# Kernel optimization log

Measured on AMD Instinct MI355X. Metric: run time of the kernel, lower is better.

## Reference

```python
import jax, jax.numpy as jnp
import numpy as np

NUM_HEADS = 16
WINDOW = 128
PERSIST = 16


def setup_inputs() -> dict:
    key = jax.random.key(0)
    ks = jax.random.split(key, 6)
    B, S, D, L = 2, 2048, 2048, 512
    sd = 1.0 / np.sqrt(D)
    sl = 1.0 / np.sqrt(L)
    return {
        "x": jax.random.normal(ks[0], (B, S, D), dtype=jnp.float32),
        "Wq": jax.random.normal(ks[1], (D, D), dtype=jnp.float32) * sd,
        "Wkv": jax.random.normal(ks[2], (D, L), dtype=jnp.float32) * sd,
        "Wk": jax.random.normal(ks[3], (L, D), dtype=jnp.float32) * sl,
        "Wv": jax.random.normal(ks[4], (L, D), dtype=jnp.float32) * sl,
        "Wo": jax.random.normal(ks[5], (D, D), dtype=jnp.float32) * sd,
    }


def reference(x, Wq, Wkv, Wk, Wv, Wo):
    B, S, D = x.shape
    H = NUM_HEADS
    hd = D // H
    scale = hd ** -0.5

    q = (x @ Wq).reshape(B, S, H, hd)
    kv_latent = x @ Wkv                      # MLA-style latent bottleneck
    k = (kv_latent @ Wk).reshape(B, S, H, hd)
    v = (kv_latent @ Wv).reshape(B, S, H, hd)

    # causal + sliding-window + persistent attention-sink mask
    qi = jnp.arange(S)[:, None]
    ki = jnp.arange(S)[None, :]
    mask = (ki <= qi) & ((qi - ki < WINDOW) | (ki < PERSIST))  # [S,S]

    scores = jnp.einsum("bqhd,bkhd->bhqk", q, k) * scale
    scores = jnp.where(mask[None, None], scores, jnp.finfo(scores.dtype).min)
    attn = jax.nn.softmax(scores, axis=-1)
    out = jnp.einsum("bhqk,bkhd->bqhd", attn, v).reshape(B, S, D)
    return out @ Wo
```

## Files before the change

kernel.cpp:

```cpp
#include <hip/hip_runtime.h>

typedef float f32x4 __attribute__((ext_vector_type(4)));
typedef __bf16 bf16x8 __attribute__((ext_vector_type(8)));

__device__ __forceinline__ short f2bf(float f) {
    union { float f; unsigned u; } x; x.f = f;
    unsigned r = x.u + 0x7fffu + ((x.u >> 16) & 1u);
    return (short)(r >> 16);
}

__device__ __forceinline__ void store_out(float* p, float v) { *p = v; }
__device__ __forceinline__ void store_out(short* p, float v) { *p = f2bf(v); }

__device__ __forceinline__ void gload_lds16(const short* g, short* l) {
    __builtin_amdgcn_global_load_lds(
        (__attribute__((address_space(1))) void*)(void*)g,
        (__attribute__((address_space(3))) void*)l, 16, 0, 0);
}

__global__ void prep_all(const float* __restrict__ x, short* __restrict__ xb,
                         const float* __restrict__ Wq, const float* __restrict__ Wo,
                         const float* __restrict__ Wk, const float* __restrict__ Wv,
                         const float* __restrict__ Wkv,
                         short* __restrict__ WqkvT, short* __restrict__ WoT,
                         short* __restrict__ WkT, short* __restrict__ WvT) {
    __shared__ float tile[32][33];
    int id = blockIdx.x;
    const int t = threadIdx.x;
    if (id < 8192) {
        const int i = id * 256 + t;
        float4 v = ((const float4*)x)[i];
        ((short4*)xb)[i] = make_short4(f2bf(v.x), f2bf(v.y), f2bf(v.z), f2bf(v.w));
        return;
    }
    id -= 8192;
    const float* in; short* out; int R, C, xt, yt;
    if (id < 4096)       { in = Wq;  out = WqkvT; R = 2048; C = 2048; xt = id & 63; yt = id >> 6; }
    else if (id < 8192)  { id -= 4096; in = Wo;  out = WoT;  R = 2048; C = 2048; xt = id & 63; yt = id >> 6; }
    else if (id < 9216)  { id -= 8192; in = Wk;  out = WkT;  R = 512;  C = 2048; xt = id & 63; yt = id >> 6; }
    else if (id < 10240) { id -= 9216; in = Wv;  out = WvT;  R = 512;  C = 2048; xt = id & 63; yt = id >> 6; }
    else                 { id -= 10240; in = Wkv; out = WqkvT + (size_t)2048 * 2048;
                           R = 2048; C = 512; xt = id & 15; yt = id >> 4; }
    const int c0 = xt * 32, r0 = yt * 32;
    const int tx = t & 31, ty = t >> 5;
#pragma unroll
    for (int i = 0; i < 32; i += 8)
        tile[ty + i][tx] = in[(size_t)(r0 + ty + i) * C + c0 + tx];
    __syncthreads();
#pragma unroll
    for (int i = 0; i < 32; i += 8)
        out[(size_t)(c0 + ty + i) * R + r0 + tx] = f2bf(tile[tx][ty + i]);
}

#define MFMA16(a, b, c) __builtin_amdgcn_mfma_f32_16x16x32_bf16(a, b, c, 0, 0, 0)

#define LBASE(buf, kh, ab) ((((((buf) << 1) | (kh)) << 1) | (ab)) * 8192)

#define STAGE(P, ld, tt, kh, buf, ab)                                   \
    do {                                                                \
        const int kb_ = (tt) * 64 + (kh) * 32;                          \
        const short* s_ = (P) + kb_;                                    \
        short* d_ = lds + LBASE(buf, kh, ab) + w * 512;                 \
        gload_lds16(s_, d_);                                            \
        gload_lds16(s_ + (size_t)128 * (ld), d_ + 4096);                \
    } while (0)

#define VM6 asm volatile("s_waitcnt vmcnt(6)" ::: "memory")

#define MM_ROW(mi, areg)                                                \
    acc[mi][0] = MFMA16(areg, bv0, acc[mi][0]);                         \
    acc[mi][1] = MFMA16(areg, bv1, acc[mi][1]);                         \
    acc[mi][2] = MFMA16(areg, bv2, acc[mi][2]);                         \
    acc[mi][3] = MFMA16(areg, bv3, acc[mi][3]);

#define HALFK(buf, kh, STG0, W0, STG1)                                  \
    {                                                                   \
        bf16x8 bv0, bv1, bv2, bv3;                                      \
        {                                                               \
            const short* Ab_ = lds + LBASE(buf, kh, 0) + (wm * 128) * 32 + foff; \
            const short* Bb_ = lds + LBASE(buf, kh, 1) + (wn * 64) * 32 + foff;  \
            bf16x8 a0_ = *(const bf16x8*)&Ab_[0];                       \
            bf16x8 a1_ = *(const bf16x8*)&Ab_[512];                     \
            bf16x8 a2_ = *(const bf16x8*)&Ab_[1024];                    \
            bf16x8 a3_ = *(const bf16x8*)&Ab_[1536];                    \
            bv0 = *(const bf16x8*)&Bb_[0];                              \
            bv1 = *(const bf16x8*)&Bb_[512];                            \
            bv2 = *(const bf16x8*)&Bb_[1024];                           \
            bv3 = *(const bf16x8*)&Bb_[1536];                           \
            STG0;                                                       \
            W0;                                                         \
            __builtin_amdgcn_s_barrier();                               \
            asm volatile("s_waitcnt lgkmcnt(0)" ::: "memory");          \
            __builtin_amdgcn_sched_barrier(0);                          \
            __builtin_amdgcn_s_setprio(1);                              \
            MM_ROW(0, a0_) MM_ROW(1, a1_) MM_ROW(2, a2_) MM_ROW(3, a3_) \
            __builtin_amdgcn_s_setprio(0);                              \
            __builtin_amdgcn_s_barrier();                               \
        }                                                               \
        {                                                               \
            const short* Ab_ = lds + LBASE(buf, kh, 0) + (wm * 128 + 64) * 32 + foff; \
            bf16x8 a0_ = *(const bf16x8*)&Ab_[0];                       \
            bf16x8 a1_ = *(const bf16x8*)&Ab_[512];                     \
            bf16x8 a2_ = *(const bf16x8*)&Ab_[1024];                    \
            bf16x8 a3_ = *(const bf16x8*)&Ab_[1536];                    \
            STG1;                                                       \
            __builtin_amdgcn_s_barrier();                               \
            asm volatile("s_waitcnt lgkmcnt(0)" ::: "memory");          \
            __builtin_amdgcn_sched_barrier(0);                          \
            __builtin_amdgcn_s_setprio(1);                              \
            MM_ROW(4, a0_) MM_ROW(5, a1_) MM_ROW(6, a2_) MM_ROW(7, a3_) \
            __builtin_amdgcn_s_setprio(0);                              \
            __builtin_amdgcn_s_barrier();                               \
        }                                                               \
    }

template <typename OutT>
__device__ __forceinline__ void gemm256_core(
    const short* __restrict__ A, const short* __restrict__ Bt, OutT* __restrict__ C,
    int m0, int n0, int K, int lda, int ldb, int ldc, short* lds) {
    const int t = threadIdx.x;
    const int w = t >> 6, l = t & 63;
    const int wm = w >> 2, wn = w & 3;
    const int l15 = l & 15, lc = l >> 4;

    const int su = (l & 7) ^ ((l >> 3) & 7);
    const int srow = (w << 4) + ((l >> 3) << 1) + (su >> 2);
    const int scol = (su & 3) << 3;
    const short* Ag = A + (size_t)(m0 + srow) * lda + scol;
    const short* Bg = Bt + (size_t)(n0 + srow) * ldb + scol;

    const int i3 = ((((l15 & 1) << 2) | lc) ^ ((l15 >> 1) & 7));
    const int foff = (l15 >> 1) * 64 + i3 * 8;

    f32x4 acc[8][4] = {};

    const int ntm1 = (K >> 6) - 1;
    const int niter = K >> 7;

    STAGE(Ag, lda, 0, 0, 0, 0);
    STAGE(Bg, ldb, 0, 0, 0, 1);
    STAGE(Ag, lda, 0, 1, 0, 0);
    STAGE(Bg, ldb, 0, 1, 0, 1);
    STAGE(Ag, lda, 1, 0, 1, 0);
    STAGE(Bg, ldb, 1, 0, 1, 1);
    asm volatile("s_waitcnt vmcnt(8)" ::: "memory");
    __builtin_amdgcn_s_barrier();

#pragma unroll 1
    for (int it = 0; it < niter; ++it) {
        const int tt = it * 2;
        const int t1 = tt + 1;
        const int t2 = (tt + 2 > ntm1) ? ntm1 : tt + 2;
        const int t3 = (tt + 3 > ntm1) ? ntm1 : tt + 3;
        HALFK(0, 0, STAGE(Ag, lda, t1, 1, 1, 0), VM6, STAGE(Bg, ldb, t1, 1, 1, 1))
        HALFK(0, 1, STAGE(Ag, lda, t2, 0, 0, 0), VM6, STAGE(Bg, ldb, t2, 0, 0, 1))
        HALFK(1, 0, STAGE(Ag, lda, t2, 1, 0, 0), VM6, STAGE(Bg, ldb, t2, 1, 0, 1))
        HALFK(1, 1, STAGE(Ag, lda, t3, 0, 1, 0), VM6, STAGE(Bg, ldb, t3, 0, 1, 1))
    }

    asm volatile("s_waitcnt vmcnt(0)" ::: "memory");

    const int crow = m0 + wm * 128 + lc * 4;
    const int ccol = n0 + wn * 64 + l15;
#pragma unroll
    for (int mi = 0; mi < 8; ++mi)
#pragma unroll
        for (int ni = 0; ni < 4; ++ni) {
            OutT* cp = C + (size_t)(crow + mi * 16) * ldc + ccol + ni * 16;
#pragma unroll
            for (int rr = 0; rr < 4; ++rr)
                store_out(cp + (size_t)rr * ldc, acc[mi][ni][rr]);
        }
}

__global__ __launch_bounds__(512, 2)
void gemm256_kv(const short* __restrict__ kvl, const short* __restrict__ WkT,
                short* __restrict__ kk, const short* __restrict__ WvT,
                short* __restrict__ vT) {
    extern __shared__ short lds[];
    int id = blockIdx.x;
    if (id < 128) {
        gemm256_core<short>(kvl, WkT, kk, (id >> 3) * 256, (id & 7) * 256,
                            512, 2560, 512, 2048, lds);
    } else {
        id -= 128;
        gemm256_core<short>(WvT, kvl, vT, (id >> 4) * 256, (id & 15) * 256,
                            512, 512, 2560, 4096, lds);
    }
}

#define LQ(s) ((s) * 13312)

#define QSTG(ps, pt)                                                    \
    do {                                                                \
        const int kb_ = (pt) * 32;                                      \
        gload_lds16(Ag + kb_, lds + LQ(ps) + w * 512);                  \
        gload_lds16(Ag + kb_ + (size_t)128 * lda, lds + LQ(ps) + 4096 + w * 512); \
        gload_lds16(Bg + kb_, lds + LQ(ps) + 8192 + w * 512);           \
        if (w < 2)                                                      \
            gload_lds16(Bh + kb_, lds + LQ(ps) + 12288 + w * 512);      \
    } while (0)

#define QPH(s, ps, pt)                                                  \
    {                                                                   \
        const short* Ab_ = lds + LQ(s) + wm * 2048 + foff;              \
        const short* Bb_ = lds + LQ(s) + 8192 + wn * 2560 + foff;       \
        bf16x8 a0_ = *(const bf16x8*)&Ab_[0];                           \
        bf16x8 a1_ = *(const bf16x8*)&Ab_[512];                         \
        bf16x8 a2_ = *(const bf16x8*)&Ab_[1024];                        \
        bf16x8 a3_ = *(const bf16x8*)&Ab_[1536];                        \
        bf16x8 b0_ = *(const bf16x8*)&Bb_[0];                           \
        bf16x8 b1_ = *(const bf16x8*)&Bb_[512];                         \
        bf16x8 b2_ = *(const bf16x8*)&Bb_[1024];                        \
        bf16x8 b3_ = *(const bf16x8*)&Bb_[1536];                        \
        bf16x8 b4_ = *(const bf16x8*)&Bb_[2048];                        \
        QSTG(ps, pt);                                                   \
        asm volatile("s_waitcnt vmcnt(8)" ::: "memory");                \
        __builtin_amdgcn_s_barrier();                                   \
        asm volatile("s_waitcnt lgkmcnt(0)" ::: "memory");              \
        __builtin_amdgcn_sched_barrier(0);                              \
        __builtin_amdgcn_s_setprio(1);                                  \
        acc[0][0]=MFMA16(a0_,b0_,acc[0][0]); acc[0][1]=MFMA16(a0_,b1_,acc[0][1]); \
        acc[0][2]=MFMA16(a0_,b2_,acc[0][2]); acc[0][3]=MFMA16(a0_,b3_,acc[0][3]); \
        acc[0][4]=MFMA16(a0_,b4_,acc[0][4]);                            \
        acc[1][0]=MFMA16(a1_,b0_,acc[1][0]); acc[1][1]=MFMA16(a1_,b1_,acc[1][1]); \
        acc[1][2]=MFMA16(a1_,b2_,acc[1][2]); acc[1][3]=MFMA16(a1_,b3_,acc[1][3]); \
        acc[1][4]=MFMA16(a1_,b4_,acc[1][4]);                            \
        acc[2][0]=MFMA16(a2_,b0_,acc[2][0]); acc[2][1]=MFMA16(a2_,b1_,acc[2][1]); \
        acc[2][2]=MFMA16(a2_,b2_,acc[2][2]); acc[2][3]=MFMA16(a2_,b3_,acc[2][3]); \
        acc[2][4]=MFMA16(a2_,b4_,acc[2][4]);                            \
        acc[3][0]=MFMA16(a3_,b0_,acc[3][0]); acc[3][1]=MFMA16(a3_,b1_,acc[3][1]); \
        acc[3][2]=MFMA16(a3_,b2_,acc[3][2]); acc[3][3]=MFMA16(a3_,b3_,acc[3][3]); \
        acc[3][4]=MFMA16(a3_,b4_,acc[3][4]);                            \
        __builtin_amdgcn_s_setprio(0);                                  \
        __builtin_amdgcn_s_barrier();                                   \
    }

__global__ __launch_bounds__(512, 1)
void gemm_qkv160(const short* __restrict__ A, const short* __restrict__ Bt,
                 short* __restrict__ C, int K, int lda, int ldb, int ldc) {
    extern __shared__ short lds[];
    const int sw = ((int)blockIdx.x & 7) * 32 + ((int)blockIdx.x >> 3);
    const int m0 = (sw >> 4) * 256, n0 = (sw & 15) * 160;
    const int t = threadIdx.x;
    const int w = t >> 6, l = t & 63;
    const int wm = w >> 1, wn = w & 1;
    const int l15 = l & 15, lc = l >> 4;

    const int su = (l & 7) ^ ((l >> 3) & 7);
    const int srow = (w << 4) + ((l >> 3) << 1) + (su >> 2);
    const int scol = (su & 3) << 3;
    const short* Ag = A + (size_t)(m0 + srow) * lda + scol;
    const short* Bg = Bt + (size_t)(n0 + srow) * ldb + scol;
    const short* Bh = Bt + (size_t)(n0 + 128 + srow) * ldb + scol;

    const int i3 = ((((l15 & 1) << 2) | lc) ^ ((l15 >> 1) & 7));
    const int foff = (l15 >> 1) * 64 + i3 * 8;

    f32x4 acc[4][5] = {};
    const int last = (K >> 5) - 1;

    QSTG(0, 0); QSTG(1, 1); QSTG(2, 2);
    asm volatile("s_waitcnt vmcnt(6)" ::: "memory");
    __builtin_amdgcn_s_barrier();

#pragma unroll 1
    for (int it = 0; it < (K >> 7); ++it) {
        const int h0 = it * 4;
        const int q3 = h0 + 3;
        const int q4 = (h0 + 4 > last) ? last : h0 + 4;
        const int q5 = (h0 + 5 > last) ? last : h0 + 5;
        const int q6 = (h0 + 6 > last) ? last : h0 + 6;
        QPH(0, 3, q3)
        QPH(1, 0, q4)
        QPH(2, 1, q5)
        QPH(3, 2, q6)
    }
    asm volatile("s_waitcnt vmcnt(0)" ::: "memory");

    const int crow = m0 + wm * 64 + lc * 4;
    const int ccol = n0 + wn * 80 + l15;
#pragma unroll
    for (int mi = 0; mi < 4; ++mi)
#pragma unroll
        for (int ni = 0; ni < 5; ++ni) {
            short* cp = C + (size_t)(crow + mi * 16) * ldc + ccol + ni * 16;
#pragma unroll
            for (int rr = 0; rr < 4; ++rr)
                store_out(cp + (size_t)rr * ldc, acc[mi][ni][rr]);
        }
}

#define LB2(s) ((s) * 12288)

#define STG2(ps, pt)                                                    \
    do {                                                                \
        const int kb_ = (pt) * 32;                                      \
        gload_lds16(Ag + kb_, lds + LB2(ps) + w * 512);                 \
        gload_lds16(Ag + kb_ + (size_t)128 * lda, lds + LB2(ps) + 4096 + w * 512); \
        gload_lds16(Bg + kb_, lds + LB2(ps) + 8192 + w * 512);          \
    } while (0)

#define PH2(s, ps, pt)                                                  \
    {                                                                   \
        const short* Ab_ = lds + LB2(s) + wm * 2048 + foff;             \
        const short* Bb_ = lds + LB2(s) + 8192 + wn * 2048 + foff;      \
        bf16x8 a0_ = *(const bf16x8*)&Ab_[0];                           \
        bf16x8 a1_ = *(const bf16x8*)&Ab_[512];                         \
        bf16x8 a2_ = *(const bf16x8*)&Ab_[1024];                        \
        bf16x8 a3_ = *(const bf16x8*)&Ab_[1536];                        \
        bf16x8 b0_ = *(const bf16x8*)&Bb_[0];                           \
        bf16x8 b1_ = *(const bf16x8*)&Bb_[512];                         \
        bf16x8 b2_ = *(const bf16x8*)&Bb_[1024];                        \
        bf16x8 b3_ = *(const bf16x8*)&Bb_[1536];                        \
        STG2(ps, pt);                                                   \
        asm volatile("s_waitcnt vmcnt(6)" ::: "memory");                \
        __builtin_amdgcn_s_barrier();                                   \
        asm volatile("s_waitcnt lgkmcnt(0)" ::: "memory");              \
        __builtin_amdgcn_sched_barrier(0);                              \
        __builtin_amdgcn_s_setprio(1);                                  \
        acc[0][0]=MFMA16(a0_,b0_,acc[0][0]); acc[0][1]=MFMA16(a0_,b1_,acc[0][1]); \
        acc[0][2]=MFMA16(a0_,b2_,acc[0][2]); acc[0][3]=MFMA16(a0_,b3_,acc[0][3]); \
        acc[1][0]=MFMA16(a1_,b0_,acc[1][0]); acc[1][1]=MFMA16(a1_,b1_,acc[1][1]); \
        acc[1][2]=MFMA16(a1_,b2_,acc[1][2]); acc[1][3]=MFMA16(a1_,b3_,acc[1][3]); \
        acc[2][0]=MFMA16(a2_,b0_,acc[2][0]); acc[2][1]=MFMA16(a2_,b1_,acc[2][1]); \
        acc[2][2]=MFMA16(a2_,b2_,acc[2][2]); acc[2][3]=MFMA16(a2_,b3_,acc[2][3]); \
        acc[3][0]=MFMA16(a3_,b0_,acc[3][0]); acc[3][1]=MFMA16(a3_,b1_,acc[3][1]); \
        acc[3][2]=MFMA16(a3_,b2_,acc[3][2]); acc[3][3]=MFMA16(a3_,b3_,acc[3][3]); \
        __builtin_amdgcn_s_setprio(0);                                  \
        __builtin_amdgcn_s_barrier();                                   \
    }

__global__ __launch_bounds__(512, 1)
void gemm_out(const short* __restrict__ A, const short* __restrict__ Bt,
              float* __restrict__ C, int K, int lda, int ldb, int ldc) {
    extern __shared__ short lds[];
    const int sw = ((int)blockIdx.x & 7) * 32 + ((int)blockIdx.x >> 3);
    const int m0 = (sw >> 4) * 256, n0 = (sw & 15) * 128;
    const int t = threadIdx.x;
    const int w = t >> 6, l = t & 63;
    const int wm = w >> 1, wn = w & 1;
    const int l15 = l & 15, lc = l >> 4;

    const int su = (l & 7) ^ ((l >> 3) & 7);
    const int srow = (w << 4) + ((l >> 3) << 1) + (su >> 2);
    const int scol = (su & 3) << 3;
    const short* Ag = A + (size_t)(m0 + srow) * lda + scol;
    const short* Bg = Bt + (size_t)(n0 + srow) * ldb + scol;

    const int i3 = ((((l15 & 1) << 2) | lc) ^ ((l15 >> 1) & 7));
    const int foff = (l15 >> 1) * 64 + i3 * 8;

    f32x4 acc[4][4] = {};

    const int nkh1 = (K >> 5) - 1;

    STG2(0, 0);
    STG2(1, 1);
    STG2(2, 2);
    asm volatile("s_waitcnt vmcnt(6)" ::: "memory");
    __builtin_amdgcn_s_barrier();

#pragma unroll 1
    for (int it = 0; it < (K >> 7); ++it) {
        const int h0 = it * 4;
        const int p3 = h0 + 3;
        const int p4 = (h0 + 4 > nkh1) ? nkh1 : h0 + 4;
        const int p5 = (h0 + 5 > nkh1) ? nkh1 : h0 + 5;
        const int p6 = (h0 + 6 > nkh1) ? nkh1 : h0 + 6;
        PH2(0, 3, p3)
        PH2(1, 0, p4)
        PH2(2, 1, p5)
        PH2(3, 2, p6)
    }

    asm volatile("s_waitcnt vmcnt(0)" ::: "memory");

    const int crow = m0 + wm * 64 + lc * 4;
    const int ccol = n0 + wn * 64 + l15;
#pragma unroll
    for (int mi = 0; mi < 4; ++mi)
#pragma unroll
        for (int ni = 0; ni < 4; ++ni) {
            float* cp = C + (size_t)(crow + mi * 16) * ldc + ccol + ni * 16;
#pragma unroll
            for (int rr = 0; rr < 4; ++rr)
                store_out(cp + (size_t)rr * ldc, acc[mi][ni][rr]);
        }
}

#define A_S 2048
#define A_D 2048
#define A_M 4096
#define A_HD 128
__global__ __launch_bounds__(256)
void attn_win3(const short* __restrict__ Q, const short* __restrict__ K,
               const short* __restrict__ vT, short* __restrict__ O, int ldq) {
    const int qt = blockIdx.x, h = blockIdx.y, b = blockIdx.z;
    const int Qs = qt * 64;
    const int t = threadIdx.x, w = t >> 6, l = t & 63;
    const int qs = Qs + w * 16;
    const int lg = l >> 4, ln = l & 15;
    const float SCALE = 0.088388347648318447f;

    __shared__ __align__(16) short sK[2][512 * 8];
    __shared__ __align__(16) short sV[2][512 * 8];
    __shared__ __align__(16) short sP[4][16][40];

    const size_t bS = (size_t)b * A_S;
    const short* qrow = Q + (bS + qs + ln) * ldq + h * A_HD;
    bf16x8 qf[4];
#pragma unroll
    for (int ks = 0; ks < 4; ++ks)
        qf[ks] = *(const bf16x8*)(qrow + ks * 32 + lg * 8);

    f32x4 o[8] = {};
    float lsum[4] = {0.f, 0.f, 0.f, 0.f};

    int C_lo = (Qs - 127) >> 5; if (C_lo < 0) C_lo = 0;
    const int C_hi = (Qs + 63) >> 5;
    const bool sink = C_lo > 0;
    const int total = (C_hi - C_lo + 1) + (sink ? 1 : 0);

    const int key0 = t >> 4, dseg0s = (t & 15) ^ (key0 & 7);
    const int d0 = t >> 2, ksg0 = (t & 3) ^ ((d0 >> 1) & 3);
    const int key1 = (256 + t) >> 4, dseg1s = (t & 15) ^ (key1 & 7);
    const int d1 = (256 + t) >> 2, ksg1 = (t & 3) ^ ((d1 >> 1) & 3);
    const short* Kb = K + bS * A_D + h * A_HD;
    const short* Vb = vT + (size_t)h * A_HD * A_M + b * A_S;

#define ASTAGE(kb, buf)                                                         \
    do {                                                                        \
        gload_lds16(Kb + (size_t)((kb) + key0) * A_D + dseg0s * 8,              \
                    &sK[buf][(size_t)(w * 64) * 8]);                            \
        gload_lds16(Vb + (size_t)d0 * A_M + (kb) + ksg0 * 8,                    \
                    &sV[buf][(size_t)(w * 64) * 8]);                            \
        gload_lds16(Kb + (size_t)((kb) + key1) * A_D + dseg1s * 8,              \
                    &sK[buf][(size_t)(256 + w * 64) * 8]);                      \
        gload_lds16(Vb + (size_t)d1 * A_M + (kb) + ksg1 * 8,                    \
                    &sV[buf][(size_t)(256 + w * 64) * 8]);                      \
    } while (0)

#define CHUNK_KB(ci) ((((sink) && (ci) == 0) ? 0 : (C_lo + (ci) - (sink ? 1 : 0))) * 32)

    ASTAGE(CHUNK_KB(0), 0);
    __syncthreads();

    for (int ci = 0; ci < total; ++ci) {
        if (ci + 1 < total) {
            const int nkb = CHUNK_KB(ci + 1);
            ASTAGE(nkb, (ci + 1) & 1);
        }
        const int kb = CHUNK_KB(ci);
        const int buf = ci & 1;
        const bool any = (kb < 16) || ((kb + 31 >= qs - 127) && (kb <= qs + 15));
        if (any) {
            f32x4 s0 = {0.f, 0.f, 0.f, 0.f}, s1 = {0.f, 0.f, 0.f, 0.f};
#pragma unroll
            for (int ks = 0; ks < 4; ++ks) {
                const int dsg = ks * 4 + lg;
                bf16x8 k0 = *(const bf16x8*)&sK[buf][(ln * 16 + (dsg ^ (ln & 7))) * 8];
                bf16x8 k1 = *(const bf16x8*)&sK[buf][((16 + ln) * 16 + (dsg ^ (ln & 7))) * 8];
                s0 = __builtin_amdgcn_mfma_f32_16x16x32_bf16(qf[ks], k0, s0, 0, 0, 0);
                s1 = __builtin_amdgcn_mfma_f32_16x16x32_bf16(qf[ks], k1, s1, 0, 0, 0);
            }
            const int k0i = kb + ln, k1i = kb + 16 + ln;
#pragma unroll
            for (int r = 0; r < 4; ++r) {
                const int qi = qs + lg * 4 + r;
                const bool m0 = (k0i <= qi) && ((qi - k0i < 128) || (k0i < 16));
                const bool m1 = (k1i <= qi) && ((qi - k1i < 128) || (k1i < 16));
                const float p0 = m0 ? __expf(s0[r] * SCALE) : 0.f;
                const float p1 = m1 ? __expf(s1[r] * SCALE) : 0.f;
                lsum[r] += p0 + p1;
                sP[w][lg * 4 + r][ln] = f2bf(p0);
                sP[w][lg * 4 + r][16 + ln] = f2bf(p1);
            }
            bf16x8 pf = *(const bf16x8*)&sP[w][ln][lg * 8];
#pragma unroll
            for (int dgi = 0; dgi < 8; ++dgi) {
                const int d = dgi * 16 + ln;
                bf16x8 vf = *(const bf16x8*)&sV[buf][(d * 4 + (lg ^ ((ln >> 1) & 3))) * 8];
                o[dgi] = __builtin_amdgcn_mfma_f32_16x16x32_bf16(pf, vf, o[dgi], 0, 0, 0);
            }
        }
        __syncthreads();
    }
#undef ASTAGE
#undef CHUNK_KB

#pragma unroll
    for (int r = 0; r < 4; ++r) {
        float s = lsum[r];
        s += __shfl_xor(s, 1); s += __shfl_xor(s, 2);
        s += __shfl_xor(s, 4); s += __shfl_xor(s, 8);
        const float inv = 1.0f / s;
        short* orow = O + (bS + qs + lg * 4 + r) * A_D + h * A_HD + ln;
#pragma unroll
        for (int dgi = 0; dgi < 8; ++dgi)
            orow[dgi * 16] = f2bf(o[dgi][r] * inv);
    }
}

extern "C" void kernel_launch(void* const* d_in, const int* in_sizes, int n_in,
                              void* d_out, int out_size, void* d_ws, size_t ws_size,
                              hipStream_t stream) {
    (void)in_sizes; (void)n_in; (void)out_size; (void)ws_size;
    const float* x   = (const float*)d_in[0];
    const float* Wq  = (const float*)d_in[1];
    const float* Wkv = (const float*)d_in[2];
    const float* Wk  = (const float*)d_in[3];
    const float* Wv  = (const float*)d_in[4];
    const float* Wo  = (const float*)d_in[5];
    float* out = (float*)d_out;

    const int B = 2, S = 2048, D = 2048, L = 512, H = 16;
    const int M = B * S;
    const int NQ = D + L;

    short* p = (short*)d_ws;
    short* xb    = p; p += (size_t)M * D;
    short* WqkvT = p; p += (size_t)NQ * D;
    short* WkT   = p; p += (size_t)D * L;
    short* WvT   = p; p += (size_t)D * L;
    short* WoT   = p; p += (size_t)D * D;
    short* qkv   = p; p += (size_t)M * NQ;
    short* kk    = p; p += (size_t)M * D;
    short* vT    = p; p += (size_t)D * M;
    short* ao    = p; p += (size_t)M * D;

    static bool attr_done = false;
    if (!attr_done) {
        hipFuncSetAttribute((const void*)&gemm256_kv,
                            hipFuncAttributeMaxDynamicSharedMemorySize, 131072);
        hipFuncSetAttribute((const void*)&gemm_qkv160,
                            hipFuncAttributeMaxDynamicSharedMemorySize, 106496);
        hipFuncSetAttribute((const void*)&gemm_out,
                            hipFuncAttributeMaxDynamicSharedMemorySize, 98304);
        attr_done = true;
    }

    prep_all<<<19456, 256, 0, stream>>>(x, xb, Wq, Wo, Wk, Wv, Wkv,
                                        WqkvT, WoT, WkT, WvT);
    gemm_qkv160<<<256, 512, 106496, stream>>>(xb, WqkvT, qkv, D, D, D, NQ);
    gemm256_kv<<<256, 512, 131072, stream>>>(qkv + D, WkT, kk, WvT, vT);

    attn_win3<<<dim3(S / 64, H, B), 256, 0, stream>>>(qkv, kk, vT, ao, NQ);

    gemm_out<<<256, 512, 98304, stream>>>(ao, WoT, out, D, D, D, D);
}
```

Measured before the change: 254.8 us.

## Move Wo transpose into attention kernel tail and drop explicit LDS waits

The Wo fp32-to-bf16 transpose leaves the prep kernel and is done by extra blocks appended to the attention grid (qt>=32), so it overlaps with the lightly loaded attention work. This is meant to shorten the serial prep phase. Separately, the explicit lgkmcnt(0) wait and sched_barrier before the MFMA bursts in two GEMM macros are removed, which leaves the compiler to schedule the LDS-read waits. That could allow better interleaving but may change ordering around the barrier.

```diff
diff --git a/kernel.cpp b/kernel.cpp
--- a/kernel.cpp
+++ b/kernel.cpp
@@ -19,10 +19,10 @@
 }
 
 __global__ void prep_all(const float* __restrict__ x, short* __restrict__ xb,
-                         const float* __restrict__ Wq, const float* __restrict__ Wo,
+                         const float* __restrict__ Wq,
                          const float* __restrict__ Wk, const float* __restrict__ Wv,
                          const float* __restrict__ Wkv,
-                         short* __restrict__ WqkvT, short* __restrict__ WoT,
+                         short* __restrict__ WqkvT,
                          short* __restrict__ WkT, short* __restrict__ WvT) {
     __shared__ float tile[32][33];
     int id = blockIdx.x;
@@ -35,12 +35,11 @@
     }
     id -= 8192;
     const float* in; short* out; int R, C, xt, yt;
-    if (id < 4096)       { in = Wq;  out = WqkvT; R = 2048; C = 2048; xt = id & 63; yt = id >> 6; }
-    else if (id < 8192)  { id -= 4096; in = Wo;  out = WoT;  R = 2048; C = 2048; xt = id & 63; yt = id >> 6; }
-    else if (id < 9216)  { id -= 8192; in = Wk;  out = WkT;  R = 512;  C = 2048; xt = id & 63; yt = id >> 6; }
-    else if (id < 10240) { id -= 9216; in = Wv;  out = WvT;  R = 512;  C = 2048; xt = id & 63; yt = id >> 6; }
-    else                 { id -= 10240; in = Wkv; out = WqkvT + (size_t)2048 * 2048;
-                           R = 2048; C = 512; xt = id & 15; yt = id >> 4; }
+    if (id < 4096)      { in = Wq;  out = WqkvT; R = 2048; C = 2048; xt = id & 63; yt = id >> 6; }
+    else if (id < 5120) { id -= 4096; in = Wk;  out = WkT;  R = 512;  C = 2048; xt = id & 63; yt = id >> 6; }
+    else if (id < 6144) { id -= 5120; in = Wv;  out = WvT;  R = 512;  C = 2048; xt = id & 63; yt = id >> 6; }
+    else                { id -= 6144; in = Wkv; out = WqkvT + (size_t)2048 * 2048;
+                          R = 2048; C = 512; xt = id & 15; yt = id >> 4; }
     const int c0 = xt * 32, r0 = yt * 32;
     const int tx = t & 31, ty = t >> 5;
 #pragma unroll
@@ -217,8 +216,6 @@
         QSTG(ps, pt);                                                   \
         asm volatile("s_waitcnt vmcnt(8)" ::: "memory");                \
         __builtin_amdgcn_s_barrier();                                   \
-        asm volatile("s_waitcnt lgkmcnt(0)" ::: "memory");              \
-        __builtin_amdgcn_sched_barrier(0);                              \
         __builtin_amdgcn_s_setprio(1);                                  \
         acc[0][0]=MFMA16(a0_,b0_,acc[0][0]); acc[0][1]=MFMA16(a0_,b1_,acc[0][1]); \
         acc[0][2]=MFMA16(a0_,b2_,acc[0][2]); acc[0][3]=MFMA16(a0_,b3_,acc[0][3]); \
@@ -316,8 +313,6 @@
         STG2(ps, pt);                                                   \
         asm volatile("s_waitcnt vmcnt(6)" ::: "memory");                \
         __builtin_amdgcn_s_barrier();                                   \
-        asm volatile("s_waitcnt lgkmcnt(0)" ::: "memory");              \
-        __builtin_amdgcn_sched_barrier(0);                              \
         __builtin_amdgcn_s_setprio(1);                                  \
         acc[0][0]=MFMA16(a0_,b0_,acc[0][0]); acc[0][1]=MFMA16(a0_,b1_,acc[0][1]); \
         acc[0][2]=MFMA16(a0_,b2_,acc[0][2]); acc[0][3]=MFMA16(a0_,b3_,acc[0][3]); \
@@ -395,17 +390,36 @@
 #define A_HD 128
 __global__ __launch_bounds__(256)
 void attn_win3(const short* __restrict__ Q, const short* __restrict__ K,
-               const short* __restrict__ vT, short* __restrict__ O, int ldq) {
+               const short* __restrict__ vT, short* __restrict__ O, int ldq,
+               const float* __restrict__ Wo, short* __restrict__ WoT) {
+    __shared__ __align__(16) short sK[2][512 * 8];
+    __shared__ __align__(16) short sV[2][512 * 8];
+    __shared__ __align__(16) short sP[4][16][40];
+
     const int qt = blockIdx.x, h = blockIdx.y, b = blockIdx.z;
+    const int t = threadIdx.x;
+
+    if (qt >= 32) {
+        const int tid = (qt - 32) * 32 + h * 2 + b;
+        const int xt = tid & 63, yt = tid >> 6;
+        const int c0 = xt * 32, r0 = yt * 32;
+        const int tx = t & 31, ty = t >> 5;
+        float (*tile)[33] = (float(*)[33])sK;
+#pragma unroll
+        for (int i = 0; i < 32; i += 8)
+            tile[ty + i][tx] = Wo[(size_t)(r0 + ty + i) * 2048 + c0 + tx];
+        __syncthreads();
+#pragma unroll
+        for (int i = 0; i < 32; i += 8)
+            WoT[(size_t)(c0 + ty + i) * 2048 + r0 + tx] = f2bf(tile[tx][ty + i]);
+        return;
+    }
+
     const int Qs = qt * 64;
-    const int t = threadIdx.x, w = t >> 6, l = t & 63;
+    const int w = t >> 6, l = t & 63;
     const int qs = Qs + w * 16;
     const int lg = l >> 4, ln = l & 15;
     const float SCALE = 0.088388347648318447f;
-
-    __shared__ __align__(16) short sK[2][512 * 8];
-    __shared__ __align__(16) short sV[2][512 * 8];
-    __shared__ __align__(16) short sP[4][16][40];
 
     const size_t bS = (size_t)b * A_S;
     const short* qrow = Q + (bS + qs + ln) * ldq + h * A_HD;
@@ -540,12 +554,12 @@
         attr_done = true;
     }
 
-    prep_all<<<19456, 256, 0, stream>>>(x, xb, Wq, Wo, Wk, Wv, Wkv,
-                                        WqkvT, WoT, WkT, WvT);
+    prep_all<<<15360, 256, 0, stream>>>(x, xb, Wq, Wk, Wv, Wkv,
+                                        WqkvT, WkT, WvT);
     gemm_qkv160<<<256, 512, 106496, stream>>>(xb, WqkvT, qkv, D, D, D, NQ);
     gemm256_kv<<<256, 512, 131072, stream>>>(qkv + D, WkT, kk, WvT, vT);
 
-    attn_win3<<<dim3(S / 64, H, B), 256, 0, stream>>>(qkv, kk, vT, ao, NQ);
+    attn_win3<<<dim3(160, H, B), 256, 0, stream>>>(qkv, kk, vT, ao, NQ, Wo, WoT);
 
     gemm_out<<<256, 512, 98304, stream>>>(ao, WoT, out, D, D, D, D);
 }
```

New measurement: 260.5 us. +2.3%, slower.
